# Optimization experiments

Measured on AMD Instinct MI355X. Metric: run time of the kernel, lower is better.

Reference implementation:

```python
import jax, jax.numpy as jnp
import numpy as np

TEMPERATURE = 0.5

def setup_inputs() -> dict:
    key = jax.random.key(0)
    k1, k2 = jax.random.split(key)
    B, D = 4096, 256
    return {
        "first_transformed": jax.random.normal(k1, (B, D), dtype=jnp.float32),
        "second_transformed": jax.random.normal(k2, (B, D), dtype=jnp.float32),
    }

def reference(first_transformed, second_transformed):
    B = first_transformed.shape[0]
    z = jnp.concatenate([first_transformed, second_transformed], axis=0)  # [2B, D]
    z = z / jnp.linalg.norm(z, axis=1, keepdims=True)
    sim = jnp.matmul(z, z.T) / TEMPERATURE  # [2B, 2B]
    n = 2 * B
    # exclude self-similarity from the denominator (mask diagonal)
    diag_mask = jnp.eye(n, dtype=bool)
    denom = jax.nn.logsumexp(jnp.where(diag_mask, -jnp.inf, sim), axis=1)  # [2B]
    # positive pair for row i is row (i+B) mod 2B
    pos_idx = (jnp.arange(n) + B) % n
    pos = sim[jnp.arange(n), pos_idx]  # [2B]
    # loss = 1/(2B) * sum_i (-log(exp(pos_i)/denom_i)) = mean(denom - pos)
    return jnp.mean(denom - pos)
```

## Files before the change

### kernel.cpp

```cpp
#include <hip/hip_runtime.h>
#include <hip/hip_bf16.h>
#include <math.h>


#define NROWS 8192
#define BHALF 4096
#define DDIM  256
#define ROWB  512
#define JT    32
#define TILEB (JT * ROWB)
#define SSTRIDE 64

#define SQRT_K1 1.6986436f
#define LN2F 0.6931471805599453f

typedef __attribute__((ext_vector_type(8))) __bf16 bf16x8;
typedef __attribute__((ext_vector_type(4))) float f32x4;

#if __has_builtin(__builtin_amdgcn_exp2f)
#define FEXP2(x) __builtin_amdgcn_exp2f(x)
#else
#define FEXP2(x) __exp2f(x)
#endif
#if __has_builtin(__builtin_amdgcn_logf)
#define FLOG2(x) __builtin_amdgcn_logf(x)
#else
#define FLOG2(x) __log2f(x)
#endif

__device__ __forceinline__ float bfu(unsigned short u) {
  union { unsigned v; float f; } x; x.v = ((unsigned)u) << 16; return x.f;
}

__global__ __launch_bounds__(256) void norm_kernel(
    const float* __restrict__ a, const float* __restrict__ b,
    char* __restrict__ zb, float* __restrict__ selfdot) {
  int row = blockIdx.x * 4 + (threadIdx.x >> 6);
  int lane = threadIdx.x & 63;
  const float* src = (row < BHALF) ? (a + (size_t)row * DDIM)
                                   : (b + (size_t)(row - BHALF) * DDIM);
  float4 v = ((const float4*)src)[lane];
  float ss = v.x * v.x + v.y * v.y + v.z * v.z + v.w * v.w;
  #pragma unroll
  for (int m = 1; m < 64; m <<= 1) ss += __shfl_xor(ss, m, 64);
  float inv = rsqrtf(ss);
  inv = inv * (1.5f - 0.5f * ss * inv * inv);
  float sc = inv * SQRT_K1;

  union { __hip_bfloat16 h; unsigned short u; } c0, c1, c2, c3;
  c0.h = __float2bfloat16(v.x * sc);
  c1.h = __float2bfloat16(v.y * sc);
  c2.h = __float2bfloat16(v.z * sc);
  c3.h = __float2bfloat16(v.w * sc);
  float q0 = bfu(c0.u), q1 = bfu(c1.u), q2 = bfu(c2.u), q3 = bfu(c3.u);
  float sq = q0 * q0 + q1 * q1 + q2 * q2 + q3 * q3;
  #pragma unroll
  for (int m = 1; m < 64; m <<= 1) sq += __shfl_xor(sq, m, 64);

  ushort4 o = make_ushort4(c0.u, c1.u, c2.u, c3.u);
  int off = row * ROWB + ((lane * 8) ^ ((row & 7) << 4));
  *(ushort4*)(zb + off) = o;
  if (lane == 0) selfdot[row] = sq;
}

__global__ __launch_bounds__(256, 3) void sim_kernel(
    const char* __restrict__ zb, float* __restrict__ s_part) {
  __shared__ __align__(16) char lds[2 * TILEB];
  __shared__ float cred[2][4][32];

  int t = blockIdx.x;
  int b = blockIdx.y;

  int wave = threadIdx.x >> 6;
  int lane = threadIdx.x & 63;
  int lrow = lane & 15;
  int kgrp = lane >> 4;
  int sw = (lrow & 7) << 4;
  int r0 = t * 128 + wave * 32;

  bf16x8 af[2][8];
  #pragma unroll
  for (int rf = 0; rf < 2; ++rf) {
    const char* rp = zb + (size_t)(r0 + rf * 16 + lrow) * ROWB;
    #pragma unroll
    for (int kk = 0; kk < 8; ++kk)
      af[rf][kk] = *(const bf16x8*)(rp + ((kk * 64 + kgrp * 16) ^ sw));
  }

  float sacc[2][4] = {};
  float cacc[2] = {};
  f32x4 C0, C1;
  bf16x8 bfv[8];

  #define STAGE_SLOT(dstbuf, colbase, i) do {                                 \
    int s_ = wave * 4 + (i);                                                  \
    const char* g_ = zb +                                                     \
        (size_t)((colbase) + (s_ >> 3) * 16 + lrow) * ROWB +                  \
        ((((s_ & 7) * 64) + kgrp * 16) ^ sw);                                 \
    char* l_ = lds + (dstbuf) * TILEB + s_ * 1024;                            \
    __builtin_amdgcn_global_load_lds(                                         \
        (const __attribute__((address_space(1))) void*)g_,                    \
        (__attribute__((address_space(3))) void*)l_, 16, 0, 0);               \
  } while (0)

  #define DSREAD(bufi, ct) do {                                               \
    const char* lbr = lds + (bufi) * TILEB + lane * 16;                       \
    _Pragma("unroll")                                                         \
    for (int kk = 0; kk < 8; ++kk)                                            \
      bfv[kk] = *(const bf16x8*)(lbr + ((ct) * 8 + kk) * 1024);               \
  } while (0)

  #define MFMA16() do {                                                       \
    C0 = (f32x4){0.f, 0.f, 0.f, 0.f};                                         \
    C1 = (f32x4){0.f, 0.f, 0.f, 0.f};                                         \
    __builtin_amdgcn_s_setprio(1);                                            \
    _Pragma("unroll")                                                         \
    for (int kk = 0; kk < 8; ++kk) {                                          \
      C0 = __builtin_amdgcn_mfma_f32_16x16x32_bf16(af[0][kk], bfv[kk], C0, 0, 0, 0); \
      C1 = __builtin_amdgcn_mfma_f32_16x16x32_bf16(af[1][kk], bfv[kk], C1, 0, 0, 0); \
    }                                                                         \
    __builtin_amdgcn_s_setprio(0);                                            \
  } while (0)

  #define FLUSHC(ct) do {                                                     \
    float cs = 0.f;                                                           \
    _Pragma("unroll")                                                         \
    for (int r = 0; r < 4; ++r) {                                             \
      float e0 = FEXP2(C0[r]), e1 = FEXP2(C1[r]);                             \
      sacc[0][r] += e0; sacc[1][r] += e1;                                     \
      cs += e0 + e1;                                                          \
    }                                                                         \
    cacc[ct] += cs;                                                           \
  } while (0)

  #define COLBASE(q) ((((t + 3 * b + ((q) >> 2)) & 63) << 7) + (((q) & 3) << 5))

  {
    int cb0 = COLBASE(0);
    #pragma unroll
    for (int i = 0; i < 4; ++i) STAGE_SLOT(0, cb0, i);
  }
  asm volatile("s_waitcnt vmcnt(0)" ::: "memory");
  __builtin_amdgcn_sched_barrier(0);
  __builtin_amdgcn_s_barrier();

  for (int jt = 0; jt < 12; ++jt) {
    int buf = jt & 1;
    int d = 3 * b + (jt >> 2);
    int u = (t + d) & 63;
    bool last = (jt == 11);
    int nextbase = last ? 0 : COLBASE(jt + 1);

    DSREAD(buf, 0);
    if (!last) {
      STAGE_SLOT(buf ^ 1, nextbase, 0);
      STAGE_SLOT(buf ^ 1, nextbase, 1);
    }
    MFMA16();
    FLUSHC(0);
    DSREAD(buf, 1);
    if (!last) {
      STAGE_SLOT(buf ^ 1, nextbase, 2);
      STAGE_SLOT(buf ^ 1, nextbase, 3);
    }
    MFMA16();
    FLUSHC(1);

    bool harvest = (d >= 1) && (d <= 31);
    if (harvest) {
      #pragma unroll
      for (int c2 = 0; c2 < 2; ++c2) {
        float v = cacc[c2];
        v += __shfl_xor(v, 16, 64);
        v += __shfl_xor(v, 32, 64);
        if (kgrp == 0) cred[jt & 1][wave][c2 * 16 + lrow] = v;
      }
    }
    cacc[0] = 0.f; cacc[1] = 0.f;

    if ((jt & 3) == 3) {
      #pragma unroll
      for (int rf = 0; rf < 2; ++rf) {
        #pragma unroll
        for (int r = 0; r < 4; ++r) {
          float v = sacc[rf][r];
          #pragma unroll
          for (int m = 1; m < 16; m <<= 1) v += __shfl_xor(v, m, 64);
          if (lrow == 0) {
            int grow = r0 + rf * 16 + kgrp * 4 + r;
            s_part[(size_t)grow * SSTRIDE + d] = v;
          }
          sacc[rf][r] = 0.f;
        }
      }
    }

    asm volatile("s_waitcnt vmcnt(0) lgkmcnt(0)" ::: "memory");
    __builtin_amdgcn_sched_barrier(0);
    __builtin_amdgcn_s_barrier();

    if (harvest && wave == (jt & 3) && lane < 32) {
      int colrow = u * 128 + (jt & 3) * 32 + lane;
      float v = cred[jt & 1][0][lane] + cred[jt & 1][1][lane] +
                cred[jt & 1][2][lane] + cred[jt & 1][3][lane];
      s_part[(size_t)colrow * SSTRIDE + 32 + d] = v;
    }
  }
  #undef COLBASE
  #undef FLUSHC
  #undef MFMA16
  #undef DSREAD
  #undef STAGE_SLOT
}

__global__ __launch_bounds__(256) void rowterm_kernel(
    const char* __restrict__ zb, const float* __restrict__ s_part,
    const float* __restrict__ selfdot, float* __restrict__ bpart) {
  int wave = threadIdx.x >> 6;
  int lane = threadIdx.x & 63;
  int rbase = blockIdx.x * 16 + wave * 4;
  float wacc = 0.f;
  #pragma unroll
  for (int rr = 0; rr < 4; ++rr) {
    int i = rbase + rr;
    int j = i ^ BHALF;
    int wo = (lane * 8) ^ ((i & 7) << 4);
    ushort4 zi = *(const ushort4*)(zb + (size_t)i * ROWB + wo);
    ushort4 zj = *(const ushort4*)(zb + (size_t)j * ROWB + wo);
    float dot = bfu(zi.x) * bfu(zj.x) + bfu(zi.y) * bfu(zj.y) +
                bfu(zi.z) * bfu(zj.z) + bfu(zi.w) * bfu(zj.w);
    float sp = s_part[(size_t)i * SSTRIDE + lane];
    #pragma unroll
    for (int m = 1; m < 64; m <<= 1) {
      dot += __shfl_xor(dot, m, 64);
      sp += __shfl_xor(sp, m, 64);
    }
    float S = sp - FEXP2(selfdot[i]);
    wacc += LN2F * (FLOG2(S) - dot);
  }
  __shared__ float red[4];
  if (lane == 0) red[wave] = wacc;
  __syncthreads();
  if (threadIdx.x == 0)
    bpart[blockIdx.x] = red[0] + red[1] + red[2] + red[3];
}

__global__ __launch_bounds__(512) void final_kernel(
    const float* __restrict__ bpart, float* __restrict__ out) {
  int t = threadIdx.x;
  float v = bpart[t];
  #pragma unroll
  for (int m = 1; m < 64; m <<= 1) v += __shfl_xor(v, m, 64);
  __shared__ float r2[8];
  if ((t & 63) == 0) r2[t >> 6] = v;
  __syncthreads();
  if (t == 0) {
    float s = 0.f;
    #pragma unroll
    for (int w = 0; w < 8; ++w) s += r2[w];
    out[0] = s / (float)NROWS;
  }
}

extern "C" void kernel_launch(void* const* d_in, const int* in_sizes, int n_in,
                              void* d_out, int out_size, void* d_ws, size_t ws_size,
                              hipStream_t stream) {
  const float* a = (const float*)d_in[0];
  const float* b = (const float*)d_in[1];
  float* out = (float*)d_out;
  char* ws = (char*)d_ws;

  char* zb = ws;
  float* selfdot = (float*)(ws + (size_t)NROWS * ROWB);
  float* s_part = selfdot + NROWS;
  float* bpart = s_part + (size_t)NROWS * SSTRIDE;

  hipLaunchKernelGGL(norm_kernel, dim3(NROWS / 4), dim3(256), 0, stream,
                     a, b, zb, selfdot);
  hipLaunchKernelGGL(sim_kernel, dim3(64, 11), dim3(256), 0, stream,
                     zb, s_part);
  hipLaunchKernelGGL(rowterm_kernel, dim3(512), dim3(256), 0, stream,
                     zb, s_part, selfdot, bpart);
  hipLaunchKernelGGL(final_kernel, dim3(1), dim3(512), 0, stream, bpart, out);
}
```

Baseline: 42.10 us.

## Switch sim kernel to 32x32x16 MFMA with a single exp pass per tile

Replaces the pairs of 16x16x32 bf16 MFMAs with 32x32x16 MFMAs and two interleaved accumulators. Each wave now computes its full 32x32 tile per column block, then applies exp2 once over 16 accumulator values instead of twice over 4+4. Row and column reductions are rewritten for the 32x32 output layout. The aim is fewer MFMA instructions and LDS reads and less exp and shuffle overhead per tile, at the cost of larger accumulator register pressure and a less interleaved mix of MFMA and exp work.

```diff
diff --git a/kernel.cpp b/kernel.cpp
--- a/kernel.cpp
+++ b/kernel.cpp
@@ -15,7 +15,7 @@
 #define LN2F 0.6931471805599453f
 
 typedef __attribute__((ext_vector_type(8))) __bf16 bf16x8;
-typedef __attribute__((ext_vector_type(4))) float f32x4;
+typedef __attribute__((ext_vector_type(16))) float f32x16;
 
 #if __has_builtin(__builtin_amdgcn_exp2f)
 #define FEXP2(x) __builtin_amdgcn_exp2f(x)
@@ -73,64 +73,46 @@
 
   int wave = threadIdx.x >> 6;
   int lane = threadIdx.x & 63;
-  int lrow = lane & 15;
-  int kgrp = lane >> 4;
-  int sw = (lrow & 7) << 4;
+  int l31 = lane & 31;
+  int lh  = lane >> 5;
+  int swz = (lane & 7) << 4;
   int r0 = t * 128 + wave * 32;
 
-  bf16x8 af[2][8];
-  #pragma unroll
-  for (int rf = 0; rf < 2; ++rf) {
-    const char* rp = zb + (size_t)(r0 + rf * 16 + lrow) * ROWB;
-    #pragma unroll
-    for (int kk = 0; kk < 8; ++kk)
-      af[rf][kk] = *(const bf16x8*)(rp + ((kk * 64 + kgrp * 16) ^ sw));
-  }
-
-  float sacc[2][4] = {};
-  float cacc[2] = {};
-  f32x4 C0, C1;
-  bf16x8 bfv[8];
+  bf16x8 af[16];
+  {
+    const char* rp = zb + (size_t)(r0 + l31) * ROWB;
+    #pragma unroll
+    for (int kk = 0; kk < 16; ++kk)
+      af[kk] = *(const bf16x8*)(rp + ((kk * 32 + lh * 16) ^ swz));
+  }
+
+  float sacc[16] = {};
+  f32x16 accA, accB;
+  bf16x8 bfv[4];
 
   #define STAGE_SLOT(dstbuf, colbase, i) do {                                 \
     int s_ = wave * 4 + (i);                                                  \
-    const char* g_ = zb +                                                     \
-        (size_t)((colbase) + (s_ >> 3) * 16 + lrow) * ROWB +                  \
-        ((((s_ & 7) * 64) + kgrp * 16) ^ sw);                                 \
+    const char* g_ = zb + (size_t)((colbase) + l31) * ROWB +                  \
+                     ((s_ * 32 + lh * 16) ^ swz);                             \
     char* l_ = lds + (dstbuf) * TILEB + s_ * 1024;                            \
     __builtin_amdgcn_global_load_lds(                                         \
         (const __attribute__((address_space(1))) void*)g_,                    \
         (__attribute__((address_space(3))) void*)l_, 16, 0, 0);               \
   } while (0)
 
-  #define DSREAD(bufi, ct) do {                                               \
-    const char* lbr = lds + (bufi) * TILEB + lane * 16;                       \
-    _Pragma("unroll")                                                         \
-    for (int kk = 0; kk < 8; ++kk)                                            \
-      bfv[kk] = *(const bf16x8*)(lbr + ((ct) * 8 + kk) * 1024);               \
-  } while (0)
-
-  #define MFMA16() do {                                                       \
-    C0 = (f32x4){0.f, 0.f, 0.f, 0.f};                                         \
-    C1 = (f32x4){0.f, 0.f, 0.f, 0.f};                                         \
+  #define CHUNK(c) do {                                                       \
+    const char* lbr = lds + buf * TILEB + lane * 16;                          \
+    bfv[0] = *(const bf16x8*)(lbr + ((c) * 4 + 0) * 1024);                    \
+    bfv[1] = *(const bf16x8*)(lbr + ((c) * 4 + 1) * 1024);                    \
+    bfv[2] = *(const bf16x8*)(lbr + ((c) * 4 + 2) * 1024);                    \
+    bfv[3] = *(const bf16x8*)(lbr + ((c) * 4 + 3) * 1024);                    \
+    if (!last) STAGE_SLOT(buf ^ 1, nextbase, c);                              \
     __builtin_amdgcn_s_setprio(1);                                            \
-    _Pragma("unroll")                                                         \
-    for (int kk = 0; kk < 8; ++kk) {                                          \
-      C0 = __builtin_amdgcn_mfma_f32_16x16x32_bf16(af[0][kk], bfv[kk], C0, 0, 0, 0); \
-      C1 = __builtin_amdgcn_mfma_f32_16x16x32_bf16(af[1][kk], bfv[kk], C1, 0, 0, 0); \
-    }                                                                         \
+    accA = __builtin_amdgcn_mfma_f32_32x32x16_bf16(af[(c)*4+0], bfv[0], accA, 0, 0, 0); \
+    accB = __builtin_amdgcn_mfma_f32_32x32x16_bf16(af[(c)*4+1], bfv[1], accB, 0, 0, 0); \
+    accA = __builtin_amdgcn_mfma_f32_32x32x16_bf16(af[(c)*4+2], bfv[2], accA, 0, 0, 0); \
+    accB = __builtin_amdgcn_mfma_f32_32x32x16_bf16(af[(c)*4+3], bfv[3], accB, 0, 0, 0); \
     __builtin_amdgcn_s_setprio(0);                                            \
-  } while (0)
-
-  #define FLUSHC(ct) do {                                                     \
-    float cs = 0.f;                                                           \
-    _Pragma("unroll")                                                         \
-    for (int r = 0; r < 4; ++r) {                                             \
-      float e0 = FEXP2(C0[r]), e1 = FEXP2(C1[r]);                             \
-      sacc[0][r] += e0; sacc[1][r] += e1;                                     \
-      cs += e0 + e1;                                                          \
-    }                                                                         \
-    cacc[ct] += cs;                                                           \
   } while (0)
 
   #define COLBASE(q) ((((t + 3 * b + ((q) >> 2)) & 63) << 7) + (((q) & 3) << 5))
@@ -151,47 +133,40 @@
     bool last = (jt == 11);
     int nextbase = last ? 0 : COLBASE(jt + 1);
 
-    DSREAD(buf, 0);
-    if (!last) {
-      STAGE_SLOT(buf ^ 1, nextbase, 0);
-      STAGE_SLOT(buf ^ 1, nextbase, 1);
-    }
-    MFMA16();
-    FLUSHC(0);
-    DSREAD(buf, 1);
-    if (!last) {
-      STAGE_SLOT(buf ^ 1, nextbase, 2);
-      STAGE_SLOT(buf ^ 1, nextbase, 3);
-    }
-    MFMA16();
-    FLUSHC(1);
+    accA = (f32x16)(0.f);
+    accB = (f32x16)(0.f);
+    CHUNK(0);
+    CHUNK(1);
+    CHUNK(2);
+    CHUNK(3);
 
     bool harvest = (d >= 1) && (d <= 31);
-    if (harvest) {
+    {
+      float cs = 0.f;
       #pragma unroll
-      for (int c2 = 0; c2 < 2; ++c2) {
-        float v = cacc[c2];
-        v += __shfl_xor(v, 16, 64);
-        v += __shfl_xor(v, 32, 64);
-        if (kgrp == 0) cred[jt & 1][wave][c2 * 16 + lrow] = v;
+      for (int r = 0; r < 16; ++r) {
+        float e = FEXP2(accA[r] + accB[r]);
+        sacc[r] += e;
+        cs += e;
       }
-    }
-    cacc[0] = 0.f; cacc[1] = 0.f;
+      cs += __shfl_xor(cs, 32, 64);
+      if (harvest && lane < 32) cred[jt & 1][wave][lane] = cs;
+    }
 
     if ((jt & 3) == 3) {
       #pragma unroll
-      for (int rf = 0; rf < 2; ++rf) {
-        #pragma unroll
-        for (int r = 0; r < 4; ++r) {
-          float v = sacc[rf][r];
-          #pragma unroll
-          for (int m = 1; m < 16; m <<= 1) v += __shfl_xor(v, m, 64);
-          if (lrow == 0) {
-            int grow = r0 + rf * 16 + kgrp * 4 + r;
-            s_part[(size_t)grow * SSTRIDE + d] = v;
-          }
-          sacc[rf][r] = 0.f;
+      for (int r = 0; r < 16; ++r) {
+        float v = sacc[r];
+        v += __shfl_xor(v, 1, 64);
+        v += __shfl_xor(v, 2, 64);
+        v += __shfl_xor(v, 4, 64);
+        v += __shfl_xor(v, 8, 64);
+        v += __shfl_xor(v, 16, 64);
+        if ((lane & 31) == 0) {
+          int grow = r0 + (r & 3) + 4 * lh + 8 * (r >> 2);
+          s_part[(size_t)grow * SSTRIDE + d] = v;
         }
+        sacc[r] = 0.f;
       }
     }
 
@@ -207,9 +182,7 @@
     }
   }
   #undef COLBASE
-  #undef FLUSHC
-  #undef MFMA16
-  #undef DSREAD
+  #undef CHUNK
   #undef STAGE_SLOT
 }
 
```

After: 64.28 us. 52.7% more time.

## Load column fragments straight from global into registers, drop LDS staging

Applied to the files above, without the earlier changes.

Removes the double-buffered LDS tile that the four waves filled cooperatively with global_load_lds. Each wave now loads its own 16-column B fragments directly from global memory into two register buffers, prefetching the next tile while it runs MFMAs on the current one. This cuts the LDS traffic, the LDS allocation and the vmcnt wait at the barrier. In exchange, global/L2 reads rise about fourfold because waves no longer share a tile, register pressure goes up, and there is less time to hide load latency.

```diff
diff --git a/kernel.cpp b/kernel.cpp
--- a/kernel.cpp
+++ b/kernel.cpp
@@ -7,8 +7,6 @@
 #define BHALF 4096
 #define DDIM  256
 #define ROWB  512
-#define JT    32
-#define TILEB (JT * ROWB)
 #define SSTRIDE 64
 
 #define SQRT_K1 1.6986436f
@@ -65,7 +63,6 @@
 
 __global__ __launch_bounds__(256, 3) void sim_kernel(
     const char* __restrict__ zb, float* __restrict__ s_part) {
-  __shared__ __align__(16) char lds[2 * TILEB];
   __shared__ float cred[2][4][32];
 
   int t = blockIdx.x;
@@ -78,46 +75,39 @@
   int sw = (lrow & 7) << 4;
   int r0 = t * 128 + wave * 32;
 
+  int koff[8];
+  #pragma unroll
+  for (int kk = 0; kk < 8; ++kk) koff[kk] = (kk * 64 + kgrp * 16) ^ sw;
+
   bf16x8 af[2][8];
   #pragma unroll
   for (int rf = 0; rf < 2; ++rf) {
     const char* rp = zb + (size_t)(r0 + rf * 16 + lrow) * ROWB;
     #pragma unroll
     for (int kk = 0; kk < 8; ++kk)
-      af[rf][kk] = *(const bf16x8*)(rp + ((kk * 64 + kgrp * 16) ^ sw));
+      af[rf][kk] = *(const bf16x8*)(rp + koff[kk]);
   }
 
   float sacc[2][4] = {};
   float cacc[2] = {};
   f32x4 C0, C1;
-  bf16x8 bfv[8];
-
-  #define STAGE_SLOT(dstbuf, colbase, i) do {                                 \
-    int s_ = wave * 4 + (i);                                                  \
-    const char* g_ = zb +                                                     \
-        (size_t)((colbase) + (s_ >> 3) * 16 + lrow) * ROWB +                  \
-        ((((s_ & 7) * 64) + kgrp * 16) ^ sw);                                 \
-    char* l_ = lds + (dstbuf) * TILEB + s_ * 1024;                            \
-    __builtin_amdgcn_global_load_lds(                                         \
-        (const __attribute__((address_space(1))) void*)g_,                    \
-        (__attribute__((address_space(3))) void*)l_, 16, 0, 0);               \
-  } while (0)
-
-  #define DSREAD(bufi, ct) do {                                               \
-    const char* lbr = lds + (bufi) * TILEB + lane * 16;                       \
+  bf16x8 bA[8], bB[8];
+
+  #define LOADF(DST, colbase, ct) do {                                        \
+    const char* rp_ = zb + (size_t)((colbase) + (ct) * 16 + lrow) * ROWB;     \
     _Pragma("unroll")                                                         \
     for (int kk = 0; kk < 8; ++kk)                                            \
-      bfv[kk] = *(const bf16x8*)(lbr + ((ct) * 8 + kk) * 1024);               \
+      DST[kk] = *(const bf16x8*)(rp_ + koff[kk]);                             \
   } while (0)
 
-  #define MFMA16() do {                                                       \
+  #define MFMA16(BV) do {                                                     \
     C0 = (f32x4){0.f, 0.f, 0.f, 0.f};                                         \
     C1 = (f32x4){0.f, 0.f, 0.f, 0.f};                                         \
     __builtin_amdgcn_s_setprio(1);                                            \
     _Pragma("unroll")                                                         \
     for (int kk = 0; kk < 8; ++kk) {                                          \
-      C0 = __builtin_amdgcn_mfma_f32_16x16x32_bf16(af[0][kk], bfv[kk], C0, 0, 0, 0); \
-      C1 = __builtin_amdgcn_mfma_f32_16x16x32_bf16(af[1][kk], bfv[kk], C1, 0, 0, 0); \
+      C0 = __builtin_amdgcn_mfma_f32_16x16x32_bf16(af[0][kk], BV[kk], C0, 0, 0, 0); \
+      C1 = __builtin_amdgcn_mfma_f32_16x16x32_bf16(af[1][kk], BV[kk], C1, 0, 0, 0); \
     }                                                                         \
     __builtin_amdgcn_s_setprio(0);                                            \
   } while (0)
@@ -135,35 +125,22 @@
 
   #define COLBASE(q) ((((t + 3 * b + ((q) >> 2)) & 63) << 7) + (((q) & 3) << 5))
 
-  {
-    int cb0 = COLBASE(0);
-    #pragma unroll
-    for (int i = 0; i < 4; ++i) STAGE_SLOT(0, cb0, i);
-  }
-  asm volatile("s_waitcnt vmcnt(0)" ::: "memory");
-  __builtin_amdgcn_sched_barrier(0);
-  __builtin_amdgcn_s_barrier();
+  LOADF(bA, COLBASE(0), 0);
 
   for (int jt = 0; jt < 12; ++jt) {
-    int buf = jt & 1;
     int d = 3 * b + (jt >> 2);
     int u = (t + d) & 63;
     bool last = (jt == 11);
-    int nextbase = last ? 0 : COLBASE(jt + 1);
-
-    DSREAD(buf, 0);
+    int colbase = COLBASE(jt);
+
+    LOADF(bB, colbase, 1);
+    MFMA16(bA);
+    FLUSHC(0);
     if (!last) {
-      STAGE_SLOT(buf ^ 1, nextbase, 0);
-      STAGE_SLOT(buf ^ 1, nextbase, 1);
-    }
-    MFMA16();
-    FLUSHC(0);
-    DSREAD(buf, 1);
-    if (!last) {
-      STAGE_SLOT(buf ^ 1, nextbase, 2);
-      STAGE_SLOT(buf ^ 1, nextbase, 3);
-    }
-    MFMA16();
+      int nb = COLBASE(jt + 1);
+      LOADF(bA, nb, 0);
+    }
+    MFMA16(bB);
     FLUSHC(1);
 
     bool harvest = (d >= 1) && (d <= 31);
@@ -195,7 +172,7 @@
       }
     }
 
-    asm volatile("s_waitcnt vmcnt(0) lgkmcnt(0)" ::: "memory");
+    asm volatile("s_waitcnt lgkmcnt(0)" ::: "memory");
     __builtin_amdgcn_sched_barrier(0);
     __builtin_amdgcn_s_barrier();
 
@@ -209,8 +186,7 @@
   #undef COLBASE
   #undef FLUSHC
   #undef MFMA16
-  #undef DSREAD
-  #undef STAGE_SLOT
+  #undef LOADF
 }
 
 __global__ __launch_bounds__(256) void rowterm_kernel(
```

Result: slower. 132.7 us (+215.1%).
